# Kernel tuning notes

Hardware: AMD Instinct MI355X
Metric: run time of the kernel (lower is better)

The kernel has to match this reference:

```python
import jax, jax.numpy as jnp
import numpy as np

T = 16384          # sequence length (bilstm_output.size(0))
HID = 256          # BiLSTM_hidden_size = 2*128
EMB = 16           # event embedding size
TMP = 128          # tmp_dim
EVENT_DIM = 2048   # event vocabulary
NEG_SLOPE = 0.01   # F.leaky_relu default


def setup_inputs() -> dict:
    key = jax.random.key(0)
    k0, k1, k2, k3 = jax.random.split(key, 4)
    def lin_w(k, out_d, in_d):
        # torch nn.Linear default init ~ U(-1/sqrt(in), 1/sqrt(in))
        bound = 1.0 / np.sqrt(in_d)
        return jax.random.uniform(k, (out_d, in_d), jnp.float32, -bound, bound)
    return {
        "bilstm_output": jax.random.normal(k0, (T, HID), jnp.float32),
        "emb_table": jax.random.normal(k1, (EVENT_DIM, EMB), jnp.float32),
        "W1": lin_w(k2, TMP, HID + EMB),
        "b1": jnp.zeros((TMP,), jnp.float32),
        "W2": lin_w(k3, EVENT_DIM, TMP),
        "b2": jnp.zeros((EVENT_DIM,), jnp.float32),
        "init_event_index": 0,
    }


def reference(bilstm_output, emb_table, W1, b1, W2, b2, init_event_index):
    # Dropout(p=0.2) is identity in eval mode.
    def step(idx, x_t):
        ev = emb_table[idx]                                  # [EMB]
        inp = jnp.concatenate([x_t, ev])                     # [HID+EMB]
        h = jax.nn.leaky_relu(inp @ W1.T + b1, negative_slope=NEG_SLOPE)  # [TMP]
        logits = h @ W2.T + b2                               # [EVENT_DIM]
        log_probs = jax.nn.log_softmax(logits)
        nxt = jnp.argmax(log_probs).astype(jnp.int32)        # greedy feedback
        return nxt, (log_probs, emb_table[nxt], nxt)

    idx0 = jnp.asarray(init_event_index, jnp.int32)
    _, (ner_output, ner_emb, ner_index) = jax.lax.scan(step, idx0, bilstm_output)
    # ner_output: [T, EVENT_DIM], ner_emb: [T, 1, EMB], ner_index: [T]
    return ner_output, ner_emb[:, None, :], ner_index
```

## Files before the change

kernel.cpp:

```cpp
#include <hip/hip_runtime.h>

#define TT 16384
#define HID 256
#define EMBD 16
#define TMPD 128
#define VOC 2048
#define NG 8
#define RPW (VOC / NG)

typedef unsigned long long u64;
typedef unsigned int u32;
typedef unsigned short u16;

#define U_OFF_B    0ull
#define C_OFF_B    8388608ull
#define SLOT_OFF_B 9437184ull

#define TAG_A 0xBEEFull
#define TAG_B 0x0000C0DEull

__global__ __launch_bounds__(128) void prep_kernel(
    const float* __restrict__ x, const float* __restrict__ emb,
    const float* __restrict__ W1, const float* __restrict__ b1,
    float* __restrict__ U, float* __restrict__ C, u64* __restrict__ slots)
{
  const int b = blockIdx.x;
  const int j = threadIdx.x;
  if (b < TT) {
    __shared__ __align__(16) float xs[HID];
    if (j < HID / 4) ((float4*)xs)[j] = ((const float4*)(x + (size_t)b * HID))[j];
    if (j < 2 * NG) slots[(size_t)b * 2 * NG + j] = ~0ull;
    __syncthreads();
    float acc = b1[j];
    const float4* wr = (const float4*)(W1 + (size_t)j * (HID + EMBD));
    #pragma unroll 8
    for (int c = 0; c < HID / 4; ++c) {
      float4 w = wr[c];
      acc = fmaf(xs[4 * c + 0], w.x, acc);
      acc = fmaf(xs[4 * c + 1], w.y, acc);
      acc = fmaf(xs[4 * c + 2], w.z, acc);
      acc = fmaf(xs[4 * c + 3], w.w, acc);
    }
    U[(size_t)b * TMPD + j] = acc;
  } else {
    const int e = b - TT;
    const float* er = emb + (size_t)e * EMBD;
    const float* wr = W1 + (size_t)j * (HID + EMBD) + HID;
    float acc = 0.f;
    #pragma unroll
    for (int k = 0; k < EMBD; ++k) acc = fmaf(er[k], wr[k], acc);
    C[(size_t)e * TMPD + j] = acc;
  }
}

__global__ __launch_bounds__(256, 1) void seq_kernel(
    const float* __restrict__ emb, const float* __restrict__ W2,
    const float* __restrict__ b2v, const int* __restrict__ init_idx,
    const float* __restrict__ U, const float* __restrict__ C,
    u64* slots,
    float* __restrict__ out0, float* __restrict__ out1,
    float* __restrict__ out2)
{
  const int g = blockIdx.x;
  const int tid = threadIdx.x;
  const int row = g * RPW + tid;

  float w[TMPD];
  {
    const float4* wr = (const float4*)(W2 + (size_t)row * TMPD);
    #pragma unroll
    for (int c = 0; c < TMPD / 4; ++c) {
      float4 v = wr[c];
      w[4 * c + 0] = v.x; w[4 * c + 1] = v.y; w[4 * c + 2] = v.z; w[4 * c + 3] = v.w;
    }
  }
  const float br = b2v[row];

  __shared__ __align__(16) float hbuf[TMPD];
  __shared__ u64 wk[4];
  __shared__ float wsum[4];
  __shared__ int bc_idx;
  __shared__ float bc_logS;

  int cur = init_idx[0];

  for (int t = 0; t < TT; ++t) {
    if (tid < TMPD) {
      float v = U[(size_t)t * TMPD + tid] + C[(size_t)cur * TMPD + tid];
      hbuf[tid] = (v > 0.f) ? v : 0.01f * v;
    }
    __syncthreads();

    float acc = br;
    #pragma unroll
    for (int k0 = 0; k0 < TMPD; k0 += 4) {
      float4 hv = *(const float4*)(hbuf + k0);
      acc = fmaf(w[k0 + 0], hv.x, acc);
      acc = fmaf(w[k0 + 1], hv.y, acc);
      acc = fmaf(w[k0 + 2], hv.z, acc);
      acc = fmaf(w[k0 + 3], hv.w, acc);
    }
    float s = __expf(acc);

    u32 fb  = __float_as_uint(acc);
    u32 ord = (fb & 0x80000000u) ? ~fb : (fb | 0x80000000u);
    u64 kk  = ((u64)ord << 32) | ((u64)(u32)(2047 - row) << 16) | TAG_A;

    #pragma unroll
    for (int off = 32; off > 0; off >>= 1) {
      u64 ok = __shfl_down(kk, off);
      float os = __shfl_down(s, off);
      s += os;
      if (ok > kk) kk = ok;
    }
    if ((tid & 63) == 0) { wk[tid >> 6] = kk; wsum[tid >> 6] = s; }
    __syncthreads();

    if (tid == 0) {
      u64 K = wk[0]; float S = wsum[0];
      #pragma unroll
      for (int q = 1; q < 4; ++q) { if (wk[q] > K) K = wk[q]; S += wsum[q]; }
      u64* base = slots + (size_t)t * 2 * NG;
      u64 keyB = ((u64)__float_as_uint(S) << 32) | TAG_B;
      __hip_atomic_store(base + 2 * g + 0, K,    __ATOMIC_RELAXED, __HIP_MEMORY_SCOPE_AGENT);
      __hip_atomic_store(base + 2 * g + 1, keyB, __ATOMIC_RELAXED, __HIP_MEMORY_SCOPE_AGENT);

      u64 ka[NG], kb[NG];
      for (;;) {
        bool okall = true;
        #pragma unroll
        for (int q = 0; q < NG; ++q) {
          ka[q] = __hip_atomic_load(base + 2 * q + 0, __ATOMIC_RELAXED, __HIP_MEMORY_SCOPE_AGENT);
          kb[q] = __hip_atomic_load(base + 2 * q + 1, __ATOMIC_RELAXED, __HIP_MEMORY_SCOPE_AGENT);
          okall &= ((ka[q] & 0xFFFFull) == TAG_A) & (((ka[q] >> 16) & 0xFFFFull) <= 2047ull);
          okall &= ((kb[q] & 0xFFFFFFFFull) == TAG_B);
        }
        if (okall) break;
      }
      u64 best = ka[0];
      float St = __uint_as_float((u32)(kb[0] >> 32));
      #pragma unroll
      for (int q = 1; q < NG; ++q) {
        St += __uint_as_float((u32)(kb[q] >> 32));
        if (ka[q] > best) best = ka[q];
      }
      bc_idx  = 2047 - (int)((best >> 16) & 0xFFFFull);
      bc_logS = __logf(St);
    }
    __syncthreads();

    const int nidx = bc_idx;
    const float lgS = bc_logS;
    out0[(size_t)t * VOC + row] = acc - lgS;
    if (g == 0) {
      if (tid < EMBD) out1[(size_t)t * EMBD + tid] = emb[(size_t)nidx * EMBD + tid];
      if (tid == 0)   out2[t] = (float)nidx;
    }
    cur = nidx;
  }
}

extern "C" void kernel_launch(void* const* d_in, const int* in_sizes, int n_in,
                              void* d_out, int out_size, void* d_ws, size_t ws_size,
                              hipStream_t stream) {
  const float* x    = (const float*)d_in[0];
  const float* emb  = (const float*)d_in[1];
  const float* W1   = (const float*)d_in[2];
  const float* b1   = (const float*)d_in[3];
  const float* W2   = (const float*)d_in[4];
  const float* b2v  = (const float*)d_in[5];
  const int*   init = (const int*)d_in[6];

  float* U    = (float*)((char*)d_ws + U_OFF_B);
  float* C    = (float*)((char*)d_ws + C_OFF_B);
  u64*   slot = (u64*)((char*)d_ws + SLOT_OFF_B);

  float* out0 = (float*)d_out;
  float* out1 = (float*)d_out + (size_t)TT * VOC;
  float* out2 = (float*)d_out + (size_t)TT * VOC + (size_t)TT * EMBD;

  hipLaunchKernelGGL(prep_kernel, dim3(TT + VOC), dim3(128), 0, stream,
                     x, emb, W1, b1, U, C, slot);
  hipLaunchKernelGGL(seq_kernel, dim3(NG), dim3(256), 0, stream,
                     emb, W2, b2v, init, U, C, slot, out0, out1, out2);
}
```

Baseline: 40.62 ms.

## Use single-wave workgroups with packed keys and all-lane polling for cross-block argmax

The sequential decode kernel now runs as 32 single-wavefront workgroups instead of 8 four-wave groups. Each wave reduces max and sum with xor shuffles and packs the value, index and an fp16 partial sum into one 64-bit slot. All lanes poll the 32 slots in parallel, which removes the intra-block shared-memory reduction and the single-thread spin loop. It also prefetches the next U row and C row and delays the embedding write. The fp16 partial sums lose precision in the log-softmax normaliser, and the smaller 5-bit tag makes stale or false matches easier.

```diff
diff --git a/kernel.cpp b/kernel.cpp
--- a/kernel.cpp
+++ b/kernel.cpp
@@ -1,12 +1,13 @@
 #include <hip/hip_runtime.h>
+#include <hip/hip_fp16.h>
 
 #define TT 16384
 #define HID 256
 #define EMBD 16
 #define TMPD 128
 #define VOC 2048
-#define NG 8
-#define RPW (VOC / NG)
+#define NWG 32
+#define RPW 64
 
 typedef unsigned long long u64;
 typedef unsigned int u32;
@@ -15,9 +16,7 @@
 #define U_OFF_B    0ull
 #define C_OFF_B    8388608ull
 #define SLOT_OFF_B 9437184ull
-
-#define TAG_A 0xBEEFull
-#define TAG_B 0x0000C0DEull
+#define TAG 0x15ull
 
 __global__ __launch_bounds__(128) void prep_kernel(
     const float* __restrict__ x, const float* __restrict__ emb,
@@ -29,7 +28,7 @@
   if (b < TT) {
     __shared__ __align__(16) float xs[HID];
     if (j < HID / 4) ((float4*)xs)[j] = ((const float4*)(x + (size_t)b * HID))[j];
-    if (j < 2 * NG) slots[(size_t)b * 2 * NG + j] = ~0ull;
+    if (j < NWG) slots[(size_t)b * NWG + j] = 0ull;
     __syncthreads();
     float acc = b1[j];
     const float4* wr = (const float4*)(W1 + (size_t)j * (HID + EMBD));
@@ -53,7 +52,7 @@
   }
 }
 
-__global__ __launch_bounds__(256, 1) void seq_kernel(
+__global__ __launch_bounds__(64, 1) void seq_kernel(
     const float* __restrict__ emb, const float* __restrict__ W2,
     const float* __restrict__ b2v, const int* __restrict__ init_idx,
     const float* __restrict__ U, const float* __restrict__ C,
@@ -62,8 +61,8 @@
     float* __restrict__ out2)
 {
   const int g = blockIdx.x;
-  const int tid = threadIdx.x;
-  const int row = g * RPW + tid;
+  const int lane = threadIdx.x;
+  const int row = (g << 6) | lane;
 
   float w[TMPD];
   {
@@ -77,18 +76,19 @@
   const float br = b2v[row];
 
   __shared__ __align__(16) float hbuf[TMPD];
-  __shared__ u64 wk[4];
-  __shared__ float wsum[4];
-  __shared__ int bc_idx;
-  __shared__ float bc_logS;
+  __shared__ __align__(16) u64 kbuf[NWG];
 
   int cur = init_idx[0];
+  float2 u2 = *(const float2*)(U + 2 * lane);
+  float2 c2 = *(const float2*)(C + (size_t)cur * TMPD + 2 * lane);
+  float2 e2 = {0.f, 0.f};
 
   for (int t = 0; t < TT; ++t) {
-    if (tid < TMPD) {
-      float v = U[(size_t)t * TMPD + tid] + C[(size_t)cur * TMPD + tid];
-      hbuf[tid] = (v > 0.f) ? v : 0.01f * v;
-    }
+    float hx = u2.x + c2.x, hy = u2.y + c2.y;
+    float2 h2 = { (hx > 0.f) ? hx : 0.01f * hx,
+                  (hy > 0.f) ? hy : 0.01f * hy };
+    *(float2*)(hbuf + 2 * lane) = h2;
+    u2 = *(const float2*)(U + (size_t)(t + 1) * TMPD + 2 * lane);
     __syncthreads();
 
     float acc = br;
@@ -102,62 +102,59 @@
     }
     float s = __expf(acc);
 
-    u32 fb  = __float_as_uint(acc);
+    float m = acc, S = s;
+    #pragma unroll
+    for (int off = 1; off < 64; off <<= 1) {
+      m = fmaxf(m, __shfl_xor(m, off));
+      S += __shfl_xor(S, off);
+    }
+    const u64 bal = __ballot(acc == m);
+    const int win = __ffsll(bal) - 1;
+    const int wrow = (g << 6) | win;
+
+    u32 fb  = __float_as_uint(m);
     u32 ord = (fb & 0x80000000u) ? ~fb : (fb | 0x80000000u);
-    u64 kk  = ((u64)ord << 32) | ((u64)(u32)(2047 - row) << 16) | TAG_A;
+    u64 key = ((u64)ord << 32) | ((u64)(u32)(2047 - wrow) << 21)
+            | ((u64)__half_as_ushort(__float2half(S)) << 5) | TAG;
 
-    #pragma unroll
-    for (int off = 32; off > 0; off >>= 1) {
-      u64 ok = __shfl_down(kk, off);
-      float os = __shfl_down(s, off);
-      s += os;
-      if (ok > kk) kk = ok;
-    }
-    if ((tid & 63) == 0) { wk[tid >> 6] = kk; wsum[tid >> 6] = s; }
+    u64* base = slots + (size_t)t * NWG;
+    if (lane == 0)
+      __hip_atomic_store(base + g, key, __ATOMIC_RELAXED, __HIP_MEMORY_SCOPE_AGENT);
+
+    u64 kq;
+    do {
+      kq = __hip_atomic_load(base + (lane & 31), __ATOMIC_RELAXED, __HIP_MEMORY_SCOPE_AGENT);
+    } while (!__all((int)((kq & 0x1Full) == TAG)));
+
+    if (lane < NWG) kbuf[lane] = kq;
     __syncthreads();
 
-    if (tid == 0) {
-      u64 K = wk[0]; float S = wsum[0];
-      #pragma unroll
-      for (int q = 1; q < 4; ++q) { if (wk[q] > K) K = wk[q]; S += wsum[q]; }
-      u64* base = slots + (size_t)t * 2 * NG;
-      u64 keyB = ((u64)__float_as_uint(S) << 32) | TAG_B;
-      __hip_atomic_store(base + 2 * g + 0, K,    __ATOMIC_RELAXED, __HIP_MEMORY_SCOPE_AGENT);
-      __hip_atomic_store(base + 2 * g + 1, keyB, __ATOMIC_RELAXED, __HIP_MEMORY_SCOPE_AGENT);
+    u64 best = kbuf[0];
+    #pragma unroll
+    for (int q = 1; q < NWG; ++q) { u64 k = kbuf[q]; if (k > best) best = k; }
+    const int nidx = 2047 - (int)((best >> 21) & 0x7FF);
 
-      u64 ka[NG], kb[NG];
-      for (;;) {
-        bool okall = true;
-        #pragma unroll
-        for (int q = 0; q < NG; ++q) {
-          ka[q] = __hip_atomic_load(base + 2 * q + 0, __ATOMIC_RELAXED, __HIP_MEMORY_SCOPE_AGENT);
-          kb[q] = __hip_atomic_load(base + 2 * q + 1, __ATOMIC_RELAXED, __HIP_MEMORY_SCOPE_AGENT);
-          okall &= ((ka[q] & 0xFFFFull) == TAG_A) & (((ka[q] >> 16) & 0xFFFFull) <= 2047ull);
-          okall &= ((kb[q] & 0xFFFFFFFFull) == TAG_B);
-        }
-        if (okall) break;
+    c2 = *(const float2*)(C + (size_t)nidx * TMPD + 2 * lane);
+
+    float Sp = 0.f;
+    #pragma unroll
+    for (int q = 0; q < NWG; ++q)
+      Sp += __half2float(__ushort_as_half((u16)((kbuf[q] >> 5) & 0xFFFFull)));
+    const float lgS = __logf(Sp);
+
+    out0[(size_t)t * VOC + row] = acc - lgS;
+
+    if (g == 0) {
+      if (lane < EMBD / 2) {
+        if (t) *(float2*)(out1 + (size_t)(t - 1) * EMBD + 2 * lane) = e2;
+        e2 = *(const float2*)(emb + (size_t)nidx * EMBD + 2 * lane);
       }
-      u64 best = ka[0];
-      float St = __uint_as_float((u32)(kb[0] >> 32));
-      #pragma unroll
-      for (int q = 1; q < NG; ++q) {
-        St += __uint_as_float((u32)(kb[q] >> 32));
-        if (ka[q] > best) best = ka[q];
-      }
-      bc_idx  = 2047 - (int)((best >> 16) & 0xFFFFull);
-      bc_logS = __logf(St);
-    }
-    __syncthreads();
-
-    const int nidx = bc_idx;
-    const float lgS = bc_logS;
-    out0[(size_t)t * VOC + row] = acc - lgS;
-    if (g == 0) {
-      if (tid < EMBD) out1[(size_t)t * EMBD + tid] = emb[(size_t)nidx * EMBD + tid];
-      if (tid == 0)   out2[t] = (float)nidx;
+      if (lane == 0) out2[t] = (float)nidx;
     }
     cur = nidx;
   }
+  if (g == 0 && lane < EMBD / 2)
+    *(float2*)(out1 + (size_t)(TT - 1) * EMBD + 2 * lane) = e2;
 }
 
 extern "C" void kernel_launch(void* const* d_in, const int* in_sizes, int n_in,
@@ -181,6 +178,6 @@
 
   hipLaunchKernelGGL(prep_kernel, dim3(TT + VOC), dim3(128), 0, stream,
                      x, emb, W1, b1, U, C, slot);
-  hipLaunchKernelGGL(seq_kernel, dim3(NG), dim3(256), 0, stream,
+  hipLaunchKernelGGL(seq_kernel, dim3(NWG), dim3(64), 0, stream,
                      emb, W2, b2v, init, U, C, slot, out0, out1, out2);
 }
```

Result: slower. 51.37 ms (+26.4%).
